# Kernel tuning notes

Measured on AMD Instinct MI355X. Metric: run time of the kernel, lower is better.

## Reference

```python
import jax, jax.numpy as jnp
import numpy as np

D_MODEL = 1024
N_HEADS = 16
D_K = D_MODEL // N_HEADS


def setup_inputs() -> dict:
    key = jax.random.key(0)
    kx, kq, kk, kv, ko = jax.random.split(key, 5)
    scale = 1.0 / np.sqrt(D_MODEL)
    return {
        "x": jax.random.normal(kx, (2, 2048, D_MODEL), dtype=jnp.float32),
        "W_Q": jax.random.normal(kq, (D_MODEL, D_MODEL), dtype=jnp.float32) * scale,
        "W_K": jax.random.normal(kk, (D_MODEL, D_MODEL), dtype=jnp.float32) * scale,
        "W_V": jax.random.normal(kv, (D_MODEL, D_MODEL), dtype=jnp.float32) * scale,
        "W_O": jax.random.normal(ko, (D_MODEL, D_MODEL), dtype=jnp.float32) * scale,
    }


def reference(x, W_Q, W_K, W_V, W_O) -> jnp.ndarray:
    B, S, _ = x.shape
    # Projections; weights stored as (d_model, d_model), applied as x @ W (Linear weight transposed convention folded into init)
    def heads(w):
        return jnp.einsum('bsd,de->bse', x, w).reshape(B, S, N_HEADS, D_K).transpose(0, 2, 1, 3)
    Q, K, V = heads(W_Q), heads(W_K), heads(W_V)  # (B,H,S,d_k)
    scores = jnp.einsum('bhqd,bhkd->bhqk', Q, K) / jnp.sqrt(jnp.asarray(D_K, x.dtype))
    causal_mask = jnp.triu(jnp.ones((S, S), dtype=bool), k=1)  # True above diagonal
    scores = jnp.where(causal_mask[None, None], jnp.asarray(-jnp.inf, x.dtype), scores)
    attn = jax.nn.softmax(scores, axis=-1)
    out = jnp.einsum('bhqk,bhkd->bhqd', attn, V)  # (B,H,S,d_k)
    out = out.transpose(0, 2, 1, 3).reshape(B, S, N_HEADS * D_K)
    return jnp.einsum('bsd,de->bse', out, W_O)
```

## Files before the change

### kernel.cpp

```cpp
#include <hip/hip_runtime.h>

typedef unsigned short u16;
typedef unsigned int u32;
typedef __attribute__((ext_vector_type(8))) __bf16 bf16x8;
typedef __attribute__((ext_vector_type(2))) __bf16 bf16x2;
typedef __attribute__((ext_vector_type(4))) float f32x4;
typedef __attribute__((ext_vector_type(16))) float f32x16;
typedef __attribute__((ext_vector_type(4))) u32 u32x4;

__device__ inline u16 f2bf(float f) {
  unsigned u = __builtin_bit_cast(unsigned, f);
  u += 0x7FFFu + ((u >> 16) & 1u);
  return (u16)(u >> 16);
}

__device__ inline u32 packbf(float a, float b) {
  bf16x2 t;
  t[0] = (__bf16)a;
  t[1] = (__bf16)b;
  return __builtin_bit_cast(u32, t);
}

__device__ inline void async16(const void* g, void* l) {
  __builtin_amdgcn_global_load_lds((const __attribute__((address_space(1))) void*)g,
                                   (__attribute__((address_space(3))) void*)l, 16, 0, 0);
}

__global__ __launch_bounds__(256) void xconv(const float* __restrict__ x, u16* __restrict__ xb) {
  int i = blockIdx.x * 256 + threadIdx.x;
  float4 v = ((const float4*)x)[i];
  ushort4 r;
  r.x = f2bf(v.x); r.y = f2bf(v.y); r.z = f2bf(v.z); r.w = f2bf(v.w);
  ((ushort4*)xb)[i] = r;
}

__global__ __launch_bounds__(256) void wtrans(const float* __restrict__ W, u16* __restrict__ Wt) {
  __shared__ u16 tile[32][33];
  const int e0 = blockIdx.x * 32;
  const int d0 = blockIdx.y * 32;
  const int tx = threadIdx.x & 31;
  const int ty = threadIdx.x >> 5;
#pragma unroll
  for (int i = ty; i < 32; i += 8)
    tile[i][tx] = f2bf(W[(size_t)(d0 + i) * 1024 + e0 + tx]);
  __syncthreads();
#pragma unroll
  for (int i = ty; i < 32; i += 8)
    Wt[(size_t)(e0 + i) * 1024 + d0 + tx] = tile[tx][i];
}

__global__ __launch_bounds__(256) void vtrans(const u16* __restrict__ QKV, u16* __restrict__ Vtg) {
  __shared__ u16 t[32][66];
  const int tid = threadIdx.x;
  const int s0 = blockIdx.x * 32, dg0 = blockIdx.y * 64, b = blockIdx.z;
  {
    const int i = tid >> 3, c = (tid & 7) * 8;
    uint4 v = *(const uint4*)(QKV + (size_t)(b * 2048 + s0 + i) * 3072 + 2048 + dg0 + c);
    u16 tmp[8];
    *(uint4*)tmp = v;
#pragma unroll
    for (int e = 0; e < 8; ++e) t[i][c + e] = tmp[e];
  }
  __syncthreads();
  {
    const int r = tid >> 2, cg = (tid & 3) * 8;
    u16 tmp[8];
#pragma unroll
    for (int e = 0; e < 8; ++e) tmp[e] = t[cg + e][r];
    *(uint4*)(Vtg + (size_t)(b * 1024 + dg0 + r) * 2048 + s0 + cg) = *(uint4*)tmp;
  }
}

template <int OUT_BF16>
__global__ __launch_bounds__(256) void gemm_bt(const u16* __restrict__ A,
                                               const u16* __restrict__ Bt,
                                               void* __restrict__ Cp,
                                               int M, int N, int K) {
  __shared__ __align__(16) u16 As[128 * 32];
  __shared__ __align__(16) u16 Bs[128 * 32];
  const int tid = threadIdx.x;
  const int lane = tid & 63;
  const int wave = tid >> 6;
  const int lr = lane & 15;
  const int lk = (lane >> 4) * 8;
  const int wm = (wave >> 1) * 64;
  const int wn = (wave & 1) * 64;
  const int bm = blockIdx.x * 128;
  const int bn = blockIdx.y * 128;
  const int srow = lane >> 2;
  const int scol = (lane & 3) * 8;

  f32x4 acc[4][4] = {};

  for (int k0 = 0; k0 < K; k0 += 32) {
#pragma unroll
    for (int r = 0; r < 2; ++r) {
      const int chunk = r * 4 + wave;
      const int row = chunk * 16 + srow;
      async16(A + (size_t)(bm + row) * K + k0 + scol, &As[chunk * 512 + lane * 8]);
      async16(Bt + (size_t)(bn + row) * K + k0 + scol, &Bs[chunk * 512 + lane * 8]);
    }
    __syncthreads();
    bf16x8 a[4], b[4];
#pragma unroll
    for (int i = 0; i < 4; ++i) {
      a[i] = *(const bf16x8*)&As[(wm + i * 16 + lr) * 32 + lk];
      b[i] = *(const bf16x8*)&Bs[(wn + i * 16 + lr) * 32 + lk];
    }
#pragma unroll
    for (int mi = 0; mi < 4; ++mi)
#pragma unroll
      for (int ni = 0; ni < 4; ++ni)
        acc[mi][ni] = __builtin_amdgcn_mfma_f32_16x16x32_bf16(a[mi], b[ni], acc[mi][ni], 0, 0, 0);
    __syncthreads();
  }

#pragma unroll
  for (int mi = 0; mi < 4; ++mi) {
#pragma unroll
    for (int ni = 0; ni < 4; ++ni) {
      const int col = bn + wn + ni * 16 + lr;
#pragma unroll
      for (int j = 0; j < 4; ++j) {
        const int row = bm + wm + mi * 16 + (lane >> 4) * 4 + j;
        if (OUT_BF16)
          ((u16*)Cp)[(size_t)row * N + col] = f2bf(acc[mi][ni][j]);
        else
          ((float*)Cp)[(size_t)row * N + col] = acc[mi][ni][j];
      }
    }
  }
}

__global__ __launch_bounds__(256) void attn_kernel(const u16* __restrict__ QKV,
                                                   const u16* __restrict__ Vtg,
                                                   u16* __restrict__ Obuf) {
  constexpr int S = 2048, LD = 3072;
  __shared__ __align__(16) u16 Ks[2][64 * 64];
  __shared__ __align__(16) u16 Vs[2][64 * 64];

  const int qt = 15 - blockIdx.x;
  const int bh = blockIdx.y;
  const int b = bh >> 4, h = bh & 15;
  const int tid = threadIdx.x, lane = tid & 63, wave = tid >> 6;
  const int l31 = lane & 31, lh = lane >> 5;

  const int qbase = qt * 128 + wave * 32;

  const u16* qrow = QKV + (size_t)(b * S + qbase + l31) * LD + h * 64;
  bf16x8 qf[4];
#pragma unroll
  for (int c = 0; c < 4; ++c) qf[c] = *(const bf16x8*)(qrow + c * 16 + lh * 8);

  const int c0 = tid, c1 = tid + 256;
  const int r0 = c0 >> 3, x0 = ((c0 & 7) ^ (r0 & 7)) << 3;
  const int r1 = c1 >> 3, x1 = ((c1 & 7) ^ (r1 & 7)) << 3;
  const u16* Kbase = QKV + (size_t)b * S * LD + 1024 + h * 64;
  const u16* Vbase = Vtg + (size_t)bh * 64 * 2048;

#define STAGE(buf, kt_)                                                          \
  do {                                                                           \
    async16(Kbase + (size_t)((kt_)*64 + r0) * LD + x0, &Ks[buf][c0 * 8]);        \
    async16(Kbase + (size_t)((kt_)*64 + r1) * LD + x1, &Ks[buf][c1 * 8]);        \
    async16(Vbase + (size_t)r0 * 2048 + (kt_)*64 + x0, &Vs[buf][c0 * 8]);        \
    async16(Vbase + (size_t)r1 * 2048 + (kt_)*64 + x1, &Vs[buf][c1 * 8]);        \
  } while (0)

  f32x16 o0 = {}, o1 = {};
  float m_run = -1e30f, l_run = 0.f;
  const float c1s = 0.18033688011112042f;

  const int nkt = 2 * qt + 2;
  const int ktlast = qbase >> 6;

  STAGE(0, 0);
  __syncthreads();

  int cur = 0;
  for (int kt = 0; kt < nkt; ++kt) {
    if (kt + 1 < nkt) STAGE(cur ^ 1, kt + 1);

    if (kt <= ktlast) {
      const u16* ks = Ks[cur];
      const u16* vs = Vs[cur];

      f32x16 t0 = {}, t1 = {};
      __builtin_amdgcn_s_setprio(1);
#pragma unroll
      for (int c = 0; c < 4; ++c) {
        const int cc = 2 * c + lh;
        const bf16x8 kf0 = *(const bf16x8*)&ks[l31 * 64 + ((cc ^ (l31 & 7)) << 3)];
        const bf16x8 kf1 = *(const bf16x8*)&ks[(32 + l31) * 64 + ((cc ^ (l31 & 7)) << 3)];
        t0 = __builtin_amdgcn_mfma_f32_32x32x16_bf16(kf0, qf[c], t0, 0, 0, 0);
        t1 = __builtin_amdgcn_mfma_f32_32x32x16_bf16(kf1, qf[c], t1, 0, 0, 0);
      }
      __builtin_amdgcn_s_setprio(0);

#pragma unroll
      for (int r = 0; r < 16; ++r) { t0[r] *= c1s; t1[r] *= c1s; }

      if (kt == ktlast) {
        const int kb = kt * 64 + 4 * lh;
        const int qa = qbase + l31;
#pragma unroll
        for (int r = 0; r < 16; ++r) {
          const int ko = (r & 3) + 8 * (r >> 2);
          if (kb + ko > qa) t0[r] = -3e38f;
          if (kb + 32 + ko > qa) t1[r] = -3e38f;
        }
      }

      float mx = fmaxf(t0[0], t1[0]);
#pragma unroll
      for (int r = 1; r < 16; ++r) mx = fmaxf(mx, fmaxf(t0[r], t1[r]));
      mx = fmaxf(mx, __shfl_xor(mx, 32));

      if (__any(mx > m_run + 8.0f)) {
        const float mnew = fmaxf(m_run, mx);
        const float scl = exp2f(m_run - mnew);
        m_run = mnew;
        l_run *= scl;
#pragma unroll
        for (int r = 0; r < 16; ++r) {
          const float sq = __shfl(scl, ((r & 3) + 8 * (r >> 2)) + 4 * lh);
          o0[r] *= sq;
          o1[r] *= sq;
        }
      }

      float ls = 0.f;
#pragma unroll
      for (int r = 0; r < 16; ++r) {
        t0[r] = exp2f(t0[r] - m_run);
        t1[r] = exp2f(t1[r] - m_run);
        ls += t0[r] + t1[r];
      }
      ls += __shfl_xor(ls, 32);
      l_run += ls;

      u32 pk0[8], pk1[8], sw0[8], sw1[8];
#pragma unroll
      for (int j = 0; j < 8; ++j) {
        pk0[j] = packbf(t0[2 * j], t0[2 * j + 1]);
        pk1[j] = packbf(t1[2 * j], t1[2 * j + 1]);
      }
#pragma unroll
      for (int j = 0; j < 8; ++j) {
        sw0[j] = __shfl_xor(pk0[j], 32);
        sw1[j] = __shfl_xor(pk1[j], 32);
      }

      __builtin_amdgcn_s_setprio(1);
#pragma unroll
      for (int kc = 0; kc < 4; ++kc) {
        const u32* pk = (kc >> 1) ? pk1 : pk0;
        const u32* sw = (kc >> 1) ? sw1 : sw0;
        const int q4 = (kc & 1) * 4;
        u32x4 wv;
        wv[0] = lh ? sw[q4 + 2] : pk[q4 + 0];
        wv[1] = lh ? sw[q4 + 3] : pk[q4 + 1];
        wv[2] = lh ? pk[q4 + 2] : sw[q4 + 0];
        wv[3] = lh ? pk[q4 + 3] : sw[q4 + 1];
        const bf16x8 pa = __builtin_bit_cast(bf16x8, wv);
        const int cc = 2 * kc + lh;
        const bf16x8 vf0 = *(const bf16x8*)&vs[l31 * 64 + ((cc ^ (l31 & 7)) << 3)];
        const bf16x8 vf1 = *(const bf16x8*)&vs[(32 + l31) * 64 + ((cc ^ (l31 & 7)) << 3)];
        o0 = __builtin_amdgcn_mfma_f32_32x32x16_bf16(pa, vf0, o0, 0, 0, 0);
        o1 = __builtin_amdgcn_mfma_f32_32x32x16_bf16(pa, vf1, o1, 0, 0, 0);
      }
      __builtin_amdgcn_s_setprio(0);
    }

    __syncthreads();
    cur ^= 1;
  }
#undef STAGE

  const float linv = 1.0f / l_run;
#pragma unroll
  for (int r = 0; r < 16; ++r) {
    const int qo = (r & 3) + 8 * (r >> 2) + 4 * lh;
    const float lq = __shfl(linv, qo);
    u16* op = Obuf + (size_t)(b * S + qbase + qo) * 1024 + h * 64 + l31;
    op[0] = f2bf(o0[r] * lq);
    op[32] = f2bf(o1[r] * lq);
  }
}

extern "C" void kernel_launch(void* const* d_in, const int* in_sizes, int n_in,
                              void* d_out, int out_size, void* d_ws, size_t ws_size,
                              hipStream_t stream) {
  const float* x  = (const float*)d_in[0];
  const float* WQ = (const float*)d_in[1];
  const float* WK = (const float*)d_in[2];
  const float* WV = (const float*)d_in[3];
  const float* WO = (const float*)d_in[4];
  float* out = (float*)d_out;

  u16* xb    = (u16*)d_ws;
  u16* WtQKV = xb + (size_t)4096 * 1024;
  u16* WtO   = WtQKV + (size_t)3072 * 1024;
  u16* QKV   = WtO + (size_t)1024 * 1024;
  u16* Obuf  = QKV + (size_t)4096 * 3072;
  u16* Vtg   = Obuf + (size_t)4096 * 1024;

  xconv<<<4096, 256, 0, stream>>>(x, xb);
  wtrans<<<dim3(32, 32), 256, 0, stream>>>(WQ, WtQKV);
  wtrans<<<dim3(32, 32), 256, 0, stream>>>(WK, WtQKV + (size_t)1024 * 1024);
  wtrans<<<dim3(32, 32), 256, 0, stream>>>(WV, WtQKV + (size_t)2048 * 1024);
  wtrans<<<dim3(32, 32), 256, 0, stream>>>(WO, WtO);

  gemm_bt<1><<<dim3(32, 24), 256, 0, stream>>>(xb, WtQKV, QKV, 4096, 3072, 1024);
  vtrans<<<dim3(64, 16, 2), 256, 0, stream>>>(QKV, Vtg);
  attn_kernel<<<dim3(16, 32), 256, 0, stream>>>(QKV, Vtg, Obuf);
  gemm_bt<0><<<dim3(32, 8), 256, 0, stream>>>(Obuf, WtO, out, 4096, 1024, 1024);
}
```

Before: 164.9 us.

## Fold softmax scale into W_Q, skip masked half-tiles, merge weight transposes

The four weight-transpose launches become one launch over a z-grid, and the softmax scale (1/sqrt(dk)*log2e) is folded into W_Q at conversion time, so the per-score multiply in attention goes away. In the attention kernel, on the diagonal tile even waves skip the upper 32-key half, which is fully masked for them, saving its QK and PV MFMAs, exp2 calls and shuffles. V is now single-buffered and loaded in the same iteration, with an explicit vmcnt wait and barrier placed between softmax and PV, which frees LDS but exposes V load latency behind the QK and softmax work. The max and sum reductions are changed to tree form. Scaling W_Q before the bf16 cast slightly changes rounding.

```diff
diff --git a/kernel.cpp b/kernel.cpp
--- a/kernel.cpp
+++ b/kernel.cpp
@@ -34,15 +34,24 @@
   ((ushort4*)xb)[i] = r;
 }
 
-__global__ __launch_bounds__(256) void wtrans(const float* __restrict__ W, u16* __restrict__ Wt) {
+__global__ __launch_bounds__(256) void wtrans4(const float* __restrict__ W0,
+                                               const float* __restrict__ W1,
+                                               const float* __restrict__ W2,
+                                               const float* __restrict__ W3,
+                                               u16* __restrict__ WtQKV,
+                                               u16* __restrict__ WtO) {
   __shared__ u16 tile[32][33];
+  const int z = blockIdx.z;
+  const float* W = (z == 0) ? W0 : (z == 1) ? W1 : (z == 2) ? W2 : W3;
+  u16* Wt = (z < 3) ? (WtQKV + (size_t)z * 1024 * 1024) : WtO;
+  const float s = (z == 0) ? 0.18033688011112042f : 1.0f;
   const int e0 = blockIdx.x * 32;
   const int d0 = blockIdx.y * 32;
   const int tx = threadIdx.x & 31;
   const int ty = threadIdx.x >> 5;
 #pragma unroll
   for (int i = ty; i < 32; i += 8)
-    tile[i][tx] = f2bf(W[(size_t)(d0 + i) * 1024 + e0 + tx]);
+    tile[i][tx] = f2bf(W[(size_t)(d0 + i) * 1024 + e0 + tx] * s);
   __syncthreads();
 #pragma unroll
   for (int i = ty; i < 32; i += 8)
@@ -137,7 +146,7 @@
                                                    u16* __restrict__ Obuf) {
   constexpr int S = 2048, LD = 3072;
   __shared__ __align__(16) u16 Ks[2][64 * 64];
-  __shared__ __align__(16) u16 Vs[2][64 * 64];
+  __shared__ __align__(16) u16 Vs[64 * 64];
 
   const int qt = 15 - blockIdx.x;
   const int bh = blockIdx.y;
@@ -158,46 +167,46 @@
   const u16* Kbase = QKV + (size_t)b * S * LD + 1024 + h * 64;
   const u16* Vbase = Vtg + (size_t)bh * 64 * 2048;
 
-#define STAGE(buf, kt_)                                                          \
-  do {                                                                           \
-    async16(Kbase + (size_t)((kt_)*64 + r0) * LD + x0, &Ks[buf][c0 * 8]);        \
-    async16(Kbase + (size_t)((kt_)*64 + r1) * LD + x1, &Ks[buf][c1 * 8]);        \
-    async16(Vbase + (size_t)r0 * 2048 + (kt_)*64 + x0, &Vs[buf][c0 * 8]);        \
-    async16(Vbase + (size_t)r1 * 2048 + (kt_)*64 + x1, &Vs[buf][c1 * 8]);        \
-  } while (0)
-
   f32x16 o0 = {}, o1 = {};
   float m_run = -1e30f, l_run = 0.f;
-  const float c1s = 0.18033688011112042f;
 
   const int nkt = 2 * qt + 2;
   const int ktlast = qbase >> 6;
 
-  STAGE(0, 0);
+  async16(Kbase + (size_t)r0 * LD + x0, &Ks[0][c0 * 8]);
+  async16(Kbase + (size_t)r1 * LD + x1, &Ks[0][c1 * 8]);
   __syncthreads();
 
   int cur = 0;
   for (int kt = 0; kt < nkt; ++kt) {
-    if (kt + 1 < nkt) STAGE(cur ^ 1, kt + 1);
-
-    if (kt <= ktlast) {
+    const bool haveNext = (kt + 1 < nkt);
+    async16(Vbase + (size_t)r0 * 2048 + kt * 64 + x0, &Vs[c0 * 8]);
+    async16(Vbase + (size_t)r1 * 2048 + kt * 64 + x1, &Vs[c1 * 8]);
+    if (haveNext) {
+      async16(Kbase + (size_t)((kt + 1) * 64 + r0) * LD + x0, &Ks[cur ^ 1][c0 * 8]);
+      async16(Kbase + (size_t)((kt + 1) * 64 + r1) * LD + x1, &Ks[cur ^ 1][c1 * 8]);
+    }
+
+    const bool active = (kt <= ktlast);
+    const bool hiA = active && ((kt < ktlast) || (wave & 1));
+
+    f32x16 t0 = {}, t1 = {};
+    u32 pk0[8], pk1[8], sw0[8], sw1[8];
+
+    if (active) {
       const u16* ks = Ks[cur];
-      const u16* vs = Vs[cur];
-
-      f32x16 t0 = {}, t1 = {};
       __builtin_amdgcn_s_setprio(1);
 #pragma unroll
       for (int c = 0; c < 4; ++c) {
         const int cc = 2 * c + lh;
         const bf16x8 kf0 = *(const bf16x8*)&ks[l31 * 64 + ((cc ^ (l31 & 7)) << 3)];
-        const bf16x8 kf1 = *(const bf16x8*)&ks[(32 + l31) * 64 + ((cc ^ (l31 & 7)) << 3)];
         t0 = __builtin_amdgcn_mfma_f32_32x32x16_bf16(kf0, qf[c], t0, 0, 0, 0);
-        t1 = __builtin_amdgcn_mfma_f32_32x32x16_bf16(kf1, qf[c], t1, 0, 0, 0);
+        if (hiA) {
+          const bf16x8 kf1 = *(const bf16x8*)&ks[(32 + l31) * 64 + ((cc ^ (l31 & 7)) << 3)];
+          t1 = __builtin_amdgcn_mfma_f32_32x32x16_bf16(kf1, qf[c], t1, 0, 0, 0);
+        }
       }
       __builtin_amdgcn_s_setprio(0);
-
-#pragma unroll
-      for (int r = 0; r < 16; ++r) { t0[r] *= c1s; t1[r] *= c1s; }
 
       if (kt == ktlast) {
         const int kb = kt * 64 + 4 * lh;
@@ -206,14 +215,18 @@
         for (int r = 0; r < 16; ++r) {
           const int ko = (r & 3) + 8 * (r >> 2);
           if (kb + ko > qa) t0[r] = -3e38f;
-          if (kb + 32 + ko > qa) t1[r] = -3e38f;
+          if (hiA && (kb + 32 + ko > qa)) t1[r] = -3e38f;
         }
       }
 
-      float mx = fmaxf(t0[0], t1[0]);
-#pragma unroll
-      for (int r = 1; r < 16; ++r) mx = fmaxf(mx, fmaxf(t0[r], t1[r]));
-      mx = fmaxf(mx, __shfl_xor(mx, 32));
+      float u[16];
+#pragma unroll
+      for (int r = 0; r < 16; ++r) u[r] = hiA ? fmaxf(t0[r], t1[r]) : t0[r];
+#pragma unroll
+      for (int s = 8; s >= 1; s >>= 1)
+#pragma unroll
+        for (int r = 0; r < s; ++r) u[r] = fmaxf(u[r], u[r + s]);
+      const float mx = fmaxf(u[0], __shfl_xor(u[0], 32));
 
       if (__any(mx > m_run + 8.0f)) {
         const float mnew = fmaxf(m_run, mx);
@@ -228,53 +241,68 @@
         }
       }
 
-      float ls = 0.f;
-#pragma unroll
-      for (int r = 0; r < 16; ++r) {
-        t0[r] = exp2f(t0[r] - m_run);
-        t1[r] = exp2f(t1[r] - m_run);
-        ls += t0[r] + t1[r];
-      }
-      ls += __shfl_xor(ls, 32);
-      l_run += ls;
-
-      u32 pk0[8], pk1[8], sw0[8], sw1[8];
-#pragma unroll
-      for (int j = 0; j < 8; ++j) {
-        pk0[j] = packbf(t0[2 * j], t0[2 * j + 1]);
-        pk1[j] = packbf(t1[2 * j], t1[2 * j + 1]);
-      }
-#pragma unroll
-      for (int j = 0; j < 8; ++j) {
-        sw0[j] = __shfl_xor(pk0[j], 32);
-        sw1[j] = __shfl_xor(pk1[j], 32);
-      }
-
+#pragma unroll
+      for (int r = 0; r < 16; ++r) t0[r] = exp2f(t0[r] - m_run);
+      if (hiA) {
+#pragma unroll
+        for (int r = 0; r < 16; ++r) t1[r] = exp2f(t1[r] - m_run);
+      }
+      float v[16];
+#pragma unroll
+      for (int r = 0; r < 16; ++r) v[r] = hiA ? (t0[r] + t1[r]) : t0[r];
+#pragma unroll
+      for (int s = 8; s >= 1; s >>= 1)
+#pragma unroll
+        for (int r = 0; r < s; ++r) v[r] += v[r + s];
+      l_run += v[0] + __shfl_xor(v[0], 32);
+
+#pragma unroll
+      for (int j = 0; j < 8; ++j) pk0[j] = packbf(t0[2 * j], t0[2 * j + 1]);
+#pragma unroll
+      for (int j = 0; j < 8; ++j) sw0[j] = __shfl_xor(pk0[j], 32);
+      if (hiA) {
+#pragma unroll
+        for (int j = 0; j < 8; ++j) pk1[j] = packbf(t1[2 * j], t1[2 * j + 1]);
+#pragma unroll
+        for (int j = 0; j < 8; ++j) sw1[j] = __shfl_xor(pk1[j], 32);
+      }
+    }
+
+    if (haveNext) asm volatile("s_waitcnt vmcnt(2)" ::: "memory");
+    else          asm volatile("s_waitcnt vmcnt(0)" ::: "memory");
+    __builtin_amdgcn_s_barrier();
+    __builtin_amdgcn_sched_barrier(0);
+
+    if (active) {
       __builtin_amdgcn_s_setprio(1);
-#pragma unroll
-      for (int kc = 0; kc < 4; ++kc) {
-        const u32* pk = (kc >> 1) ? pk1 : pk0;
-        const u32* sw = (kc >> 1) ? sw1 : sw0;
-        const int q4 = (kc & 1) * 4;
-        u32x4 wv;
-        wv[0] = lh ? sw[q4 + 2] : pk[q4 + 0];
-        wv[1] = lh ? sw[q4 + 3] : pk[q4 + 1];
-        wv[2] = lh ? pk[q4 + 2] : sw[q4 + 0];
-        wv[3] = lh ? pk[q4 + 3] : sw[q4 + 1];
-        const bf16x8 pa = __builtin_bit_cast(bf16x8, wv);
-        const int cc = 2 * kc + lh;
-        const bf16x8 vf0 = *(const bf16x8*)&vs[l31 * 64 + ((cc ^ (l31 & 7)) << 3)];
-        const bf16x8 vf1 = *(const bf16x8*)&vs[(32 + l31) * 64 + ((cc ^ (l31 & 7)) << 3)];
-        o0 = __builtin_amdgcn_mfma_f32_32x32x16_bf16(pa, vf0, o0, 0, 0, 0);
-        o1 = __builtin_amdgcn_mfma_f32_32x32x16_bf16(pa, vf1, o1, 0, 0, 0);
-      }
+#define PVSTEP(kc, pk, sw)                                                             \
+      {                                                                                \
+        const int q4 = ((kc) & 1) * 4;                                                 \
+        u32x4 wv;                                                                      \
+        wv[0] = lh ? sw[q4 + 2] : pk[q4 + 0];                                          \
+        wv[1] = lh ? sw[q4 + 3] : pk[q4 + 1];                                          \
+        wv[2] = lh ? pk[q4 + 2] : sw[q4 + 0];                                          \
+        wv[3] = lh ? pk[q4 + 3] : sw[q4 + 1];                                          \
+        const bf16x8 pa = __builtin_bit_cast(bf16x8, wv);                              \
+        const int cc = 2 * (kc) + lh;                                                  \
+        const bf16x8 vf0 = *(const bf16x8*)&Vs[l31 * 64 + ((cc ^ (l31 & 7)) << 3)];    \
+        const bf16x8 vf1 = *(const bf16x8*)&Vs[(32 + l31) * 64 + ((cc ^ (l31 & 7)) << 3)]; \
+        o0 = __builtin_amdgcn_mfma_f32_32x32x16_bf16(pa, vf0, o0, 0, 0, 0);            \
+        o1 = __builtin_amdgcn_mfma_f32_32x32x16_bf16(pa, vf1, o1, 0, 0, 0);            \
+      }
+      PVSTEP(0, pk0, sw0)
+      PVSTEP(1, pk0, sw0)
+      if (hiA) {
+        PVSTEP(2, pk1, sw1)
+        PVSTEP(3, pk1, sw1)
+      }
+#undef PVSTEP
       __builtin_amdgcn_s_setprio(0);
     }
 
     __syncthreads();
     cur ^= 1;
   }
-#undef STAGE
 
   const float linv = 1.0f / l_run;
 #pragma unroll
@@ -305,10 +333,7 @@
   u16* Vtg   = Obuf + (size_t)4096 * 1024;
 
   xconv<<<4096, 256, 0, stream>>>(x, xb);
-  wtrans<<<dim3(32, 32), 256, 0, stream>>>(WQ, WtQKV);
-  wtrans<<<dim3(32, 32), 256, 0, stream>>>(WK, WtQKV + (size_t)1024 * 1024);
-  wtrans<<<dim3(32, 32), 256, 0, stream>>>(WV, WtQKV + (size_t)2048 * 1024);
-  wtrans<<<dim3(32, 32), 256, 0, stream>>>(WO, WtO);
+  wtrans4<<<dim3(32, 32, 4), 256, 0, stream>>>(WQ, WK, WV, WO, WtQKV, WtO);
 
   gemm_bt<1><<<dim3(32, 24), 256, 0, stream>>>(xb, WtQKV, QKV, 4096, 3072, 1024);
   vtrans<<<dim3(64, 16, 2), 256, 0, stream>>>(QKV, Vtg);
```

New measurement: 170.6 us. 1.03x slower.
